# Kernel tuning notes

Hardware: AMD Instinct MI355X
Metric: run time of the kernel (lower is better)

Reference implementation:

```python
import jax, jax.numpy as jnp
import numpy as np

ETA = 0.1
DT = 1.0
H, DH = 8, 64


def setup_inputs() -> dict:
    key = jax.random.key(0)
    ks = jax.random.split(key, 7)
    B, N, D = 4, 2048, 1024
    s = 0.02
    return {
        "x": jax.random.normal(ks[0], (B, N, D), dtype=jnp.float32),
        "gamma": jax.random.uniform(ks[1], (B, N), dtype=jnp.float32),
        "state": jnp.zeros((B, H, DH, DH), dtype=jnp.float32),
        "Wq": (jax.random.normal(ks[2], (D, H * DH), dtype=jnp.float32) * s),
        "Wk": (jax.random.normal(ks[3], (D, H * DH), dtype=jnp.float32) * s),
        "Wv": (jax.random.normal(ks[4], (D, H * DH), dtype=jnp.float32) * s),
        "Wo": (jax.random.normal(ks[5], (H * DH, D), dtype=jnp.float32) * s),
        "bo": jnp.zeros((D,), dtype=jnp.float32),
    }


def reference(x, gamma, state, Wq, Wk, Wv, Wo, bo):
    B, N, D = x.shape
    # projections -> (N, B, H, DH) for scan over time
    q = (x @ Wq).reshape(B, N, H, DH).transpose(1, 0, 2, 3)
    k = (x @ Wk).reshape(B, N, H, DH).transpose(1, 0, 2, 3)
    v = (x @ Wv).reshape(B, N, H, DH).transpose(1, 0, 2, 3)
    # decay = exp(-clamp(gamma*dt, max=10)) -> (N, B)
    decay = jnp.exp(-jnp.minimum(gamma * DT, 10.0)).T

    def step(st, inp):
        q_t, k_t, v_t, d_t = inp  # (B,H,DH),(B,H,DH),(B,H,DH),(B,)
        # W_new = exp(-Gamma*dt) * stop_grad(W_old) + eta * k^T v
        st_new = d_t[:, None, None, None] * jax.lax.stop_gradient(st) \
                 + ETA * jnp.einsum('bhi,bhj->bhij', k_t, v_t)
        y_t = jnp.einsum('bhij,bhj->bhi', st_new, q_t)  # (B,H,DH)
        return st_new, y_t

    state_final, ys = jax.lax.scan(step, state, (q, k, v, decay))
    # ys: (N, B, H, DH) -> (B, N, H*DH)
    y = ys.transpose(1, 0, 2, 3).reshape(B, N, H * DH)
    out = y @ Wo + bo
    return out, state_final
```

## Files before the change

### kernel.cpp

```cpp
#include <hip/hip_runtime.h>

#define ETA 0.1f
#define BATCH 4
#define SEQ 2048
#define DMODEL 1024
#define NH 8
#define DHEAD 64
#define HD 512
#define QKVW 1536
#define CH 64
#define NCH (SEQ / CH)

typedef float f32x4 __attribute__((ext_vector_type(4)));
typedef short short8 __attribute__((ext_vector_type(8)));
typedef short short4v __attribute__((ext_vector_type(4)));

static __device__ __forceinline__ ushort f2bf(float f) {
  union { float f; unsigned u; } x; x.f = f;
  unsigned r = (x.u + 0x7fffu + ((x.u >> 16) & 1u)) >> 16;
  return (ushort)r;
}
static __device__ __forceinline__ float bf2f(ushort u) {
  union { unsigned u; float f; } x; x.u = ((unsigned)u) << 16;
  return x.f;
}

#define GLDS16(g, l)                                                    \
  __builtin_amdgcn_global_load_lds(                                     \
      (const __attribute__((address_space(1))) unsigned int*)(const void*)(g), \
      (__attribute__((address_space(3))) unsigned int*)(void*)(l), 16, 0, 0)

__global__ __launch_bounds__(256) void convx_kernel(
    const float* __restrict__ x, ushort* __restrict__ xb) {
  size_t i = ((size_t)blockIdx.x * 256 + threadIdx.x) * 16;
  ushort t[16];
#pragma unroll
  for (int u = 0; u < 4; ++u) {
    f32x4 v = *(const f32x4*)&x[i + u * 4];
#pragma unroll
    for (int e = 0; e < 4; ++e) t[u * 4 + e] = f2bf(v[e]);
  }
  *(short8*)&xb[i] = *(short8*)&t[0];
  *(short8*)&xb[i + 8] = *(short8*)&t[8];
}

__global__ __launch_bounds__(256) void convw_kernel(
    const float* __restrict__ Wq, const float* __restrict__ Wk,
    const float* __restrict__ Wv, const float* __restrict__ Wo,
    ushort* __restrict__ Wt, ushort* __restrict__ Wot) {
  const int m = blockIdx.y;
  const int bx = blockIdx.x;
  const int tid = threadIdx.x;
  __shared__ float T[32][33];

  const float* src;
  ushort* dst;
  int srcN, dstK, k0, n0, rowOff;
  if (m < 3) {
    src = (m == 0) ? Wq : ((m == 1) ? Wk : Wv);
    srcN = 512; dstK = 1024;
    k0 = (bx >> 4) << 5; n0 = (bx & 15) << 5;
    dst = Wt; rowOff = m * 512;
  } else {
    src = Wo; srcN = 1024; dstK = 512;
    k0 = (bx >> 5) << 5; n0 = (bx & 31) << 5;
    dst = Wot; rowOff = 0;
  }
  const int r = tid >> 3, c4 = (tid & 7) << 2;
  f32x4 v = *(const f32x4*)&src[(size_t)(k0 + r) * srcN + n0 + c4];
  T[r][c4 + 0] = v[0]; T[r][c4 + 1] = v[1];
  T[r][c4 + 2] = v[2]; T[r][c4 + 3] = v[3];
  __syncthreads();
  short4v o;
#pragma unroll
  for (int e = 0; e < 4; ++e) o[e] = (short)f2bf(T[c4 + e][r]);
  *(short4v*)&dst[(size_t)(rowOff + n0 + r) * dstK + k0 + c4] = o;
}

template <bool OUT_BF16>
__global__ __launch_bounds__(256) void gemm_bt_kernel(
    const ushort* __restrict__ A, const ushort* __restrict__ Bt,
    void* __restrict__ Cv, const float* __restrict__ bias,
    int M, int N, int K) {
  const int tiles_n = N >> 7;
  const int bm = blockIdx.x / tiles_n;
  const int bn = blockIdx.x % tiles_n;
  const int tid = threadIdx.x;
  const int w = tid >> 6, lane = tid & 63;
  const int wr = w >> 1, wc = w & 1;
  const int fr = lane & 15, fq = lane >> 4;

  __shared__ ushort As[2][128][32];
  __shared__ ushort Bs[2][128][32];

  f32x4 acc[4][4];
#pragma unroll
  for (int mi = 0; mi < 4; ++mi)
#pragma unroll
    for (int ni = 0; ni < 4; ++ni) acc[mi][ni] = f32x4{0.f, 0.f, 0.f, 0.f};

  const int lw = lane >> 2;
  const int lc = (lane & 3) << 3;
  const ushort* ga = A + (size_t)(bm * 128 + w * 32 + lw) * K + lc;
  const ushort* gb = Bt + (size_t)(bn * 128 + w * 32 + lw) * K + lc;
  const size_t rstep = (size_t)16 * K;

  const int nt = K >> 5;

  {
    ushort* la = &As[0][w * 32][0];
    ushort* lb = &Bs[0][w * 32][0];
    GLDS16(ga, la);
    GLDS16(ga + rstep, la + 16 * 32);
    GLDS16(gb, lb);
    GLDS16(gb + rstep, lb + 16 * 32);
  }
  asm volatile("s_waitcnt vmcnt(0)" ::: "memory");
  __syncthreads();

  for (int t = 0; t < nt; ++t) {
    if (t + 1 < nt) {
      const int nb = (t + 1) & 1;
      const int kt = (t + 1) << 5;
      ushort* la = &As[nb][w * 32][0];
      ushort* lb = &Bs[nb][w * 32][0];
      GLDS16(ga + kt, la);
      GLDS16(ga + kt + rstep, la + 16 * 32);
      GLDS16(gb + kt, lb);
      GLDS16(gb + kt + rstep, lb + 16 * 32);
    }
    const int cb = t & 1;
    short8 a[4], b[4];
#pragma unroll
    for (int mi = 0; mi < 4; ++mi)
      a[mi] = *(const short8*)&As[cb][wr * 64 + mi * 16 + fr][fq * 8];
#pragma unroll
    for (int ni = 0; ni < 4; ++ni)
      b[ni] = *(const short8*)&Bs[cb][wc * 64 + ni * 16 + fr][fq * 8];
#pragma unroll
    for (int mi = 0; mi < 4; ++mi)
#pragma unroll
      for (int ni = 0; ni < 4; ++ni)
        acc[mi][ni] = __builtin_amdgcn_mfma_f32_16x16x32_bf16(
            a[mi], b[ni], acc[mi][ni], 0, 0, 0);
    asm volatile("s_waitcnt vmcnt(0)" ::: "memory");
    __syncthreads();
  }

#pragma unroll
  for (int ni = 0; ni < 4; ++ni) {
    const int gc = bn * 128 + wc * 64 + ni * 16 + fr;
    float badd = (!OUT_BF16 && bias) ? bias[gc] : 0.f;
#pragma unroll
    for (int mi = 0; mi < 4; ++mi) {
#pragma unroll
      for (int r = 0; r < 4; ++r) {
        const int gr = bm * 128 + wr * 64 + mi * 16 + fq * 4 + r;
        if (OUT_BF16) {
          ((ushort*)Cv)[(size_t)gr * N + gc] = f2bf(acc[mi][ni][r]);
        } else {
          ((float*)Cv)[(size_t)gr * N + gc] = acc[mi][ni][r] + badd;
        }
      }
    }
  }
}

__global__ __launch_bounds__(256) void intra_kernel(
    const ushort* __restrict__ qkv, const float* __restrict__ gamma,
    ushort* __restrict__ ybf, float* __restrict__ S, float* __restrict__ clb) {
  const int bx = blockIdx.x;
  const int c = bx & (NCH - 1);
  const int h = (bx >> 5) & (NH - 1);
  const int b = bx >> 8;
  const int tid = threadIdx.x;
  const int w = tid >> 6, lane = tid & 63;
  const int fr = lane & 15, fq = lane >> 4;

  __shared__ ushort Qs[64][72];
  __shared__ ushort Vs[64][72];
  __shared__ ushort KT[64][72];
  __shared__ ushort VT[64][72];
  __shared__ ushort Ps[64][72];
  __shared__ float cumS[64];
  __shared__ float clS;

  const int p = tid >> 2, d0 = (tid & 3) * 16;
  const ushort* base = &qkv[((size_t)b * SEQ + c * CH + p) * QKVW + h * 64 + d0];
  short8 q0 = *(const short8*)base;
  short8 q1 = *(const short8*)(base + 8);
  short8 k0 = *(const short8*)(base + 512);
  short8 k1 = *(const short8*)(base + 520);
  short8 v0 = *(const short8*)(base + 1024);
  short8 v1 = *(const short8*)(base + 1032);

  if (tid < 64) {
    float g = gamma[(size_t)b * SEQ + c * CH + tid];
    float prod = expf(-fminf(g, 10.f));
#pragma unroll
    for (int off = 1; off < 64; off <<= 1) {
      float o = __shfl_up(prod, off);
      if (tid >= off) prod *= o;
    }
    cumS[tid] = prod;
    if (tid == 63) clS = prod;
  }
  __syncthreads();

  {
    const float cp = cumS[p];
    const float rc = 1.f / cp;
    ushort tq[16], tv[16];
#pragma unroll
    for (int j = 0; j < 8; ++j) {
      tq[j]     = f2bf(bf2f((ushort)q0[j]) * cp);
      tq[8 + j] = f2bf(bf2f((ushort)q1[j]) * cp);
      tv[j]     = f2bf(bf2f((ushort)v0[j]) * rc);
      tv[8 + j] = f2bf(bf2f((ushort)v1[j]) * rc);
      KT[d0 + j][p] = (ushort)k0[j];
      KT[d0 + 8 + j][p] = (ushort)k1[j];
      VT[d0 + j][p] = tv[j];
      VT[d0 + 8 + j][p] = tv[8 + j];
    }
    *(short8*)&Qs[p][d0] = *(short8*)&tq[0];
    *(short8*)&Qs[p][d0 + 8] = *(short8*)&tq[8];
    *(short8*)&Vs[p][d0] = *(short8*)&tv[0];
    *(short8*)&Vs[p][d0 + 8] = *(short8*)&tv[8];
  }
  __syncthreads();

  const int arow = w * 16 + fr;
  {
    short8 a0 = *(const short8*)&Qs[arow][fq * 8];
    short8 a1 = *(const short8*)&Qs[arow][32 + fq * 8];
#pragma unroll
    for (int cf = 0; cf < 4; ++cf) {
      f32x4 acc = {0.f, 0.f, 0.f, 0.f};
      if (cf <= w) {
        short8 b0 = *(const short8*)&Vs[cf * 16 + fr][fq * 8];
        short8 b1 = *(const short8*)&Vs[cf * 16 + fr][32 + fq * 8];
        acc = __builtin_amdgcn_mfma_f32_16x16x32_bf16(a0, b0, acc, 0, 0, 0);
        acc = __builtin_amdgcn_mfma_f32_16x16x32_bf16(a1, b1, acc, 0, 0, 0);
      }
#pragma unroll
      for (int r = 0; r < 4; ++r) {
        int pi = w * 16 + fq * 4 + r, si = cf * 16 + fr;
        Ps[pi][si] = f2bf((si <= pi) ? acc[r] * ETA : 0.f);
      }
    }
  }
  __syncthreads();

  {
    short8 p0 = *(const short8*)&Ps[arow][fq * 8];
    short8 p1 = *(const short8*)&Ps[arow][32 + fq * 8];
    short8 ka0 = *(const short8*)&KT[arow][fq * 8];
    short8 ka1 = *(const short8*)&KT[arow][32 + fq * 8];
    const float scl = ETA * clS;
    const size_t yrow0 = (size_t)b * SEQ + c * CH;
    float* Sp = &S[(((size_t)(b * NH + h)) * NCH + c) << 12];
#pragma unroll
    for (int cf = 0; cf < 4; ++cf) {
      short8 bk0 = *(const short8*)&KT[cf * 16 + fr][fq * 8];
      short8 bk1 = *(const short8*)&KT[cf * 16 + fr][32 + fq * 8];
      f32x4 accY = {0.f, 0.f, 0.f, 0.f};
      accY = __builtin_amdgcn_mfma_f32_16x16x32_bf16(p0, bk0, accY, 0, 0, 0);
      accY = __builtin_amdgcn_mfma_f32_16x16x32_bf16(p1, bk1, accY, 0, 0, 0);
      short8 bv0 = *(const short8*)&VT[cf * 16 + fr][fq * 8];
      short8 bv1 = *(const short8*)&VT[cf * 16 + fr][32 + fq * 8];
      f32x4 accS = {0.f, 0.f, 0.f, 0.f};
      accS = __builtin_amdgcn_mfma_f32_16x16x32_bf16(ka0, bv0, accS, 0, 0, 0);
      accS = __builtin_amdgcn_mfma_f32_16x16x32_bf16(ka1, bv1, accS, 0, 0, 0);
#pragma unroll
      for (int r = 0; r < 4; ++r) {
        int row = w * 16 + fq * 4 + r;
        int col = cf * 16 + fr;
        ybf[(yrow0 + row) * HD + h * 64 + col] = f2bf(accY[r]);
        Sp[row * 64 + col] = accS[r] * scl;
      }
    }
  }
  if (tid == 0 && h == 0) clb[b * NCH + c] = clS;
}

__global__ __launch_bounds__(256) void prop_kernel(
    const float* __restrict__ state0, const float* __restrict__ S,
    const float* __restrict__ clb, float* __restrict__ stash,
    float* __restrict__ state_out) {
  const int bh = blockIdx.x >> 2, rg = blockIdx.x & 3;
  const int b = bh >> 3;
  const int tid = threadIdx.x;
  const int i = rg * 16 + (tid >> 4);
  const int j0 = (tid & 15) * 4;
  const size_t off = ((size_t)bh * 64 + i) * 64 + j0;
  const size_t coff = (size_t)i * 64 + j0;

  f32x4 st = *(const f32x4*)&state0[off];
#pragma unroll 4
  for (int c = 0; c < NCH; ++c) {
    const size_t base = (((size_t)bh * NCH + c) << 12) + coff;
    *(f32x4*)&stash[base] = st;
    f32x4 s = *(const f32x4*)&S[base];
    float clv = clb[b * NCH + c];
    st = st * clv + s;
  }
  *(f32x4*)&state_out[off] = st;
}

__global__ __launch_bounds__(256) void inter_kernel(
    const ushort* __restrict__ qkv, const float* __restrict__ gamma,
    const float* __restrict__ stash, ushort* __restrict__ ybf) {
  const int bx = blockIdx.x;
  const int c = bx & (NCH - 1);
  const int h = (bx >> 5) & (NH - 1);
  const int b = bx >> 8;
  const int tid = threadIdx.x;
  const int w = tid >> 6, lane = tid & 63;
  const int fr = lane & 15, fq = lane >> 4;

  __shared__ ushort Qs[64][72];
  __shared__ ushort Bs[64][72];
  __shared__ float cumS[64];

  const int p = tid >> 2, d0 = (tid & 3) * 16;
  const ushort* qp = &qkv[((size_t)b * SEQ + c * CH + p) * QKVW + h * 64 + d0];
  short8 q0 = *(const short8*)qp;
  short8 q1 = *(const short8*)(qp + 8);
  const size_t sb = ((((size_t)(b * NH + h)) * NCH + c) << 12) + (size_t)p * 64 + d0;
  f32x4 sr[4];
#pragma unroll
  for (int u = 0; u < 4; ++u) sr[u] = *(const f32x4*)&stash[sb + u * 4];

  if (tid < 64) {
    float g = gamma[(size_t)b * SEQ + c * CH + tid];
    float prod = expf(-fminf(g, 10.f));
#pragma unroll
    for (int off = 1; off < 64; off <<= 1) {
      float o = __shfl_up(prod, off);
      if (tid >= off) prod *= o;
    }
    cumS[tid] = prod;
  }
  __syncthreads();

  {
    const float cp = cumS[p];
    ushort tq[16], ts[16];
#pragma unroll
    for (int j = 0; j < 8; ++j) {
      tq[j]     = f2bf(bf2f((ushort)q0[j]) * cp);
      tq[8 + j] = f2bf(bf2f((ushort)q1[j]) * cp);
    }
#pragma unroll
    for (int u = 0; u < 4; ++u)
#pragma unroll
      for (int e = 0; e < 4; ++e) ts[u * 4 + e] = f2bf(sr[u][e]);
    *(short8*)&Qs[p][d0] = *(short8*)&tq[0];
    *(short8*)&Qs[p][d0 + 8] = *(short8*)&tq[8];
    *(short8*)&Bs[p][d0] = *(short8*)&ts[0];
    *(short8*)&Bs[p][d0 + 8] = *(short8*)&ts[8];
  }
  __syncthreads();

  const int arow = w * 16 + fr;
  short8 a0 = *(const short8*)&Qs[arow][fq * 8];
  short8 a1 = *(const short8*)&Qs[arow][32 + fq * 8];
  const size_t yrow0 = (size_t)b * SEQ + c * CH;
#pragma unroll
  for (int cf = 0; cf < 4; ++cf) {
    short8 b0 = *(const short8*)&Bs[cf * 16 + fr][fq * 8];
    short8 b1 = *(const short8*)&Bs[cf * 16 + fr][32 + fq * 8];
    f32x4 acc = {0.f, 0.f, 0.f, 0.f};
    acc = __builtin_amdgcn_mfma_f32_16x16x32_bf16(a0, b0, acc, 0, 0, 0);
    acc = __builtin_amdgcn_mfma_f32_16x16x32_bf16(a1, b1, acc, 0, 0, 0);
#pragma unroll
    for (int r = 0; r < 4; ++r) {
      int row = w * 16 + fq * 4 + r;
      int col = cf * 16 + fr;
      size_t idx = (yrow0 + row) * HD + h * 64 + col;
      ybf[idx] = f2bf(bf2f(ybf[idx]) + acc[r]);
    }
  }
}

extern "C" void kernel_launch(void* const* d_in, const int* in_sizes, int n_in,
                              void* d_out, int out_size, void* d_ws, size_t ws_size,
                              hipStream_t stream) {
  const float* x      = (const float*)d_in[0];
  const float* gamma  = (const float*)d_in[1];
  const float* state0 = (const float*)d_in[2];
  const float* Wq     = (const float*)d_in[3];
  const float* Wk     = (const float*)d_in[4];
  const float* Wv     = (const float*)d_in[5];
  const float* Wo     = (const float*)d_in[6];
  const float* bo     = (const float*)d_in[7];

  float* out = (float*)d_out;
  float* state_out = out + (size_t)BATCH * SEQ * DMODEL;

  const int M = BATCH * SEQ;

  ushort* xb  = (ushort*)d_ws;
  ushort* wt  = xb + (size_t)M * DMODEL;
  ushort* wot = wt + (size_t)QKVW * DMODEL;
  ushort* qkv = wot + (size_t)DMODEL * HD;
  ushort* ybf = qkv + (size_t)M * QKVW;
  float*  Sb  = (float*)(ybf + (size_t)M * HD);
  float* stash = Sb + (size_t)BATCH * NH * NCH * 4096;
  float* clb   = stash + (size_t)BATCH * NH * NCH * 4096;

  dim3 blk(256);

  convx_kernel<<<dim3((M * DMODEL) / (256 * 16)), blk, 0, stream>>>(x, xb);
  convw_kernel<<<dim3(512, 4), blk, 0, stream>>>(Wq, Wk, Wv, Wo, wt, wot);

  gemm_bt_kernel<true><<<dim3((M / 128) * (QKVW / 128)), blk, 0, stream>>>(
      xb, wt, qkv, nullptr, M, QKVW, DMODEL);

  intra_kernel<<<dim3(BATCH * NH * NCH), blk, 0, stream>>>(
      qkv, gamma, ybf, Sb, clb);
  prop_kernel<<<dim3(BATCH * NH * 4), blk, 0, stream>>>(
      state0, Sb, clb, stash, state_out);
  inter_kernel<<<dim3(BATCH * NH * NCH), blk, 0, stream>>>(
      qkv, gamma, stash, ybf);

  gemm_bt_kernel<false><<<dim3((M / 128) * (DMODEL / 128)), blk, 0, stream>>>(
      ybf, wot, out, bo, M, DMODEL, HD);
}
```

Measured before the change: 100.2 us.

## Widen GEMM tiles to 128x256 with 512 threads, swizzle blocks, store chunk states in bf16

After: 99.15 us. Within noise of the previous version (-1.0%).

```diff
diff --git a/kernel.cpp b/kernel.cpp
--- a/kernel.cpp
+++ b/kernel.cpp
@@ -78,20 +78,23 @@
 }
 
 template <bool OUT_BF16>
-__global__ __launch_bounds__(256) void gemm_bt_kernel(
+__global__ __launch_bounds__(512, 4) void gemm_bt_kernel(
     const ushort* __restrict__ A, const ushort* __restrict__ Bt,
     void* __restrict__ Cv, const float* __restrict__ bias,
     int M, int N, int K) {
-  const int tiles_n = N >> 7;
-  const int bm = blockIdx.x / tiles_n;
-  const int bn = blockIdx.x % tiles_n;
+  const int tiles_n = N >> 8;
+  const int nwg = gridDim.x;
+  const int bid = blockIdx.x;
+  const int swz = (bid & 7) * (nwg >> 3) + (bid >> 3);
+  const int bm = swz / tiles_n;
+  const int bn = swz % tiles_n;
   const int tid = threadIdx.x;
   const int w = tid >> 6, lane = tid & 63;
-  const int wr = w >> 1, wc = w & 1;
+  const int wr = w >> 2, wc = w & 3;
   const int fr = lane & 15, fq = lane >> 4;
 
   __shared__ ushort As[2][128][32];
-  __shared__ ushort Bs[2][128][32];
+  __shared__ ushort Bs[2][256][32];
 
   f32x4 acc[4][4];
 #pragma unroll
@@ -99,21 +102,20 @@
 #pragma unroll
     for (int ni = 0; ni < 4; ++ni) acc[mi][ni] = f32x4{0.f, 0.f, 0.f, 0.f};
 
-  const int lw = lane >> 2;
-  const int lc = (lane & 3) << 3;
-  const ushort* ga = A + (size_t)(bm * 128 + w * 32 + lw) * K + lc;
-  const ushort* gb = Bt + (size_t)(bn * 128 + w * 32 + lw) * K + lc;
-  const size_t rstep = (size_t)16 * K;
+  const int sr = tid >> 2;
+  const int sc = (tid & 3) << 3;
+  const ushort* ga  = A  + (size_t)(bm * 128 + sr) * K + sc;
+  const ushort* gb0 = Bt + (size_t)(bn * 256 + sr) * K + sc;
+  const ushort* gb1 = Bt + (size_t)(bn * 256 + 128 + sr) * K + sc;
 
   const int nt = K >> 5;
 
   {
-    ushort* la = &As[0][w * 32][0];
-    ushort* lb = &Bs[0][w * 32][0];
+    ushort* la = &As[0][0][0] + (size_t)tid * 8;
+    ushort* lb = &Bs[0][0][0] + (size_t)tid * 8;
     GLDS16(ga, la);
-    GLDS16(ga + rstep, la + 16 * 32);
-    GLDS16(gb, lb);
-    GLDS16(gb + rstep, lb + 16 * 32);
+    GLDS16(gb0, lb);
+    GLDS16(gb1, lb + 4096);
   }
   asm volatile("s_waitcnt vmcnt(0)" ::: "memory");
   __syncthreads();
@@ -122,12 +124,11 @@
     if (t + 1 < nt) {
       const int nb = (t + 1) & 1;
       const int kt = (t + 1) << 5;
-      ushort* la = &As[nb][w * 32][0];
-      ushort* lb = &Bs[nb][w * 32][0];
+      ushort* la = &As[nb][0][0] + (size_t)tid * 8;
+      ushort* lb = &Bs[nb][0][0] + (size_t)tid * 8;
       GLDS16(ga + kt, la);
-      GLDS16(ga + kt + rstep, la + 16 * 32);
-      GLDS16(gb + kt, lb);
-      GLDS16(gb + kt + rstep, lb + 16 * 32);
+      GLDS16(gb0 + kt, lb);
+      GLDS16(gb1 + kt, lb + 4096);
     }
     const int cb = t & 1;
     short8 a[4], b[4];
@@ -149,7 +150,7 @@
 
 #pragma unroll
   for (int ni = 0; ni < 4; ++ni) {
-    const int gc = bn * 128 + wc * 64 + ni * 16 + fr;
+    const int gc = bn * 256 + wc * 64 + ni * 16 + fr;
     float badd = (!OUT_BF16 && bias) ? bias[gc] : 0.f;
 #pragma unroll
     for (int mi = 0; mi < 4; ++mi) {
@@ -168,7 +169,7 @@
 
 __global__ __launch_bounds__(256) void intra_kernel(
     const ushort* __restrict__ qkv, const float* __restrict__ gamma,
-    ushort* __restrict__ ybf, float* __restrict__ S, float* __restrict__ clb) {
+    ushort* __restrict__ ybf, ushort* __restrict__ S, float* __restrict__ clb) {
   const int bx = blockIdx.x;
   const int c = bx & (NCH - 1);
   const int h = (bx >> 5) & (NH - 1);
@@ -258,7 +259,7 @@
     short8 ka1 = *(const short8*)&KT[arow][32 + fq * 8];
     const float scl = ETA * clS;
     const size_t yrow0 = (size_t)b * SEQ + c * CH;
-    float* Sp = &S[(((size_t)(b * NH + h)) * NCH + c) << 12];
+    ushort* Sp = &S[(((size_t)(b * NH + h)) * NCH + c) << 12];
 #pragma unroll
     for (int cf = 0; cf < 4; ++cf) {
       short8 bk0 = *(const short8*)&KT[cf * 16 + fr][fq * 8];
@@ -276,7 +277,7 @@
         int row = w * 16 + fq * 4 + r;
         int col = cf * 16 + fr;
         ybf[(yrow0 + row) * HD + h * 64 + col] = f2bf(accY[r]);
-        Sp[row * 64 + col] = accS[r] * scl;
+        Sp[row * 64 + col] = f2bf(accS[r] * scl);
       }
     }
   }
@@ -284,8 +285,8 @@
 }
 
 __global__ __launch_bounds__(256) void prop_kernel(
-    const float* __restrict__ state0, const float* __restrict__ S,
-    const float* __restrict__ clb, float* __restrict__ stash,
+    const float* __restrict__ state0, const ushort* __restrict__ S,
+    const float* __restrict__ clb, ushort* __restrict__ stash,
     float* __restrict__ state_out) {
   const int bh = blockIdx.x >> 2, rg = blockIdx.x & 3;
   const int b = bh >> 3;
@@ -299,17 +300,21 @@
 #pragma unroll 4
   for (int c = 0; c < NCH; ++c) {
     const size_t base = (((size_t)bh * NCH + c) << 12) + coff;
-    *(f32x4*)&stash[base] = st;
-    f32x4 s = *(const f32x4*)&S[base];
+    short4v sv;
+#pragma unroll
+    for (int e = 0; e < 4; ++e) sv[e] = (short)f2bf(st[e]);
+    *(short4v*)&stash[base] = sv;
+    short4v s = *(const short4v*)&S[base];
     float clv = clb[b * NCH + c];
-    st = st * clv + s;
+#pragma unroll
+    for (int e = 0; e < 4; ++e) st[e] = st[e] * clv + bf2f((ushort)s[e]);
   }
   *(f32x4*)&state_out[off] = st;
 }
 
 __global__ __launch_bounds__(256) void inter_kernel(
     const ushort* __restrict__ qkv, const float* __restrict__ gamma,
-    const float* __restrict__ stash, ushort* __restrict__ ybf) {
+    const ushort* __restrict__ stash, ushort* __restrict__ ybf) {
   const int bx = blockIdx.x;
   const int c = bx & (NCH - 1);
   const int h = (bx >> 5) & (NH - 1);
@@ -327,9 +332,8 @@
   short8 q0 = *(const short8*)qp;
   short8 q1 = *(const short8*)(qp + 8);
   const size_t sb = ((((size_t)(b * NH + h)) * NCH + c) << 12) + (size_t)p * 64 + d0;
-  f32x4 sr[4];
-#pragma unroll
-  for (int u = 0; u < 4; ++u) sr[u] = *(const f32x4*)&stash[sb + u * 4];
+  short8 s0 = *(const short8*)&stash[sb];
+  short8 s1 = *(const short8*)&stash[sb + 8];
 
   if (tid < 64) {
     float g = gamma[(size_t)b * SEQ + c * CH + tid];
@@ -345,20 +349,16 @@
 
   {
     const float cp = cumS[p];
-    ushort tq[16], ts[16];
+    ushort tq[16];
 #pragma unroll
     for (int j = 0; j < 8; ++j) {
       tq[j]     = f2bf(bf2f((ushort)q0[j]) * cp);
       tq[8 + j] = f2bf(bf2f((ushort)q1[j]) * cp);
     }
-#pragma unroll
-    for (int u = 0; u < 4; ++u)
-#pragma unroll
-      for (int e = 0; e < 4; ++e) ts[u * 4 + e] = f2bf(sr[u][e]);
     *(short8*)&Qs[p][d0] = *(short8*)&tq[0];
     *(short8*)&Qs[p][d0 + 8] = *(short8*)&tq[8];
-    *(short8*)&Bs[p][d0] = *(short8*)&ts[0];
-    *(short8*)&Bs[p][d0 + 8] = *(short8*)&ts[8];
+    *(short8*)&Bs[p][d0] = s0;
+    *(short8*)&Bs[p][d0 + 8] = s1;
   }
   __syncthreads();
 
@@ -405,16 +405,17 @@
   ushort* wot = wt + (size_t)QKVW * DMODEL;
   ushort* qkv = wot + (size_t)DMODEL * HD;
   ushort* ybf = qkv + (size_t)M * QKVW;
-  float*  Sb  = (float*)(ybf + (size_t)M * HD);
-  float* stash = Sb + (size_t)BATCH * NH * NCH * 4096;
-  float* clb   = stash + (size_t)BATCH * NH * NCH * 4096;
+  ushort* Sb  = ybf + (size_t)M * HD;
+  ushort* stash = Sb + (size_t)BATCH * NH * NCH * 4096;
+  float*  clb   = (float*)(stash + (size_t)BATCH * NH * NCH * 4096);
 
   dim3 blk(256);
+  dim3 blkg(512);
 
   convx_kernel<<<dim3((M * DMODEL) / (256 * 16)), blk, 0, stream>>>(x, xb);
   convw_kernel<<<dim3(512, 4), blk, 0, stream>>>(Wq, Wk, Wv, Wo, wt, wot);
 
-  gemm_bt_kernel<true><<<dim3((M / 128) * (QKVW / 128)), blk, 0, stream>>>(
+  gemm_bt_kernel<true><<<dim3((M / 128) * (QKVW / 256)), blkg, 0, stream>>>(
       xb, wt, qkv, nullptr, M, QKVW, DMODEL);
 
   intra_kernel<<<dim3(BATCH * NH * NCH), blk, 0, stream>>>(
@@ -424,6 +425,6 @@
   inter_kernel<<<dim3(BATCH * NH * NCH), blk, 0, stream>>>(
       qkv, gamma, stash, ybf);
 
-  gemm_bt_kernel<false><<<dim3((M / 128) * (DMODEL / 128)), blk, 0, stream>>>(
+  gemm_bt_kernel<false><<<dim3((M / 128) * (DMODEL / 256)), blkg, 0, stream>>>(
       ybf, wot, out, bo, M, DMODEL, HD);
 }
```
